# Optimization experiments

Hardware: AMD Instinct MI355X
Metric: run time of the kernel (lower is better)

Reference implementation:

```python
import jax, jax.numpy as jnp
import numpy as np

N_NODES = 50000
N_EDGES = 800000
HID = 256
OUT = 128
NEG_SLOPE = 0.2


def gat_layer(x, src, dst, W_src, W_dst, a_src_vec, a_dst_vec, bias, n_nodes):
    # Dense projections (PyG lin_src / lin_dst for tuple in_channels)
    h_src = x @ W_src              # [N, C]
    h_dst = x @ W_dst              # [N, C]
    # Per-node attention logits (att_src/att_dst dot products)
    a_src = h_src @ a_src_vec      # [N]
    a_dst = h_dst @ a_dst_vec      # [N]
    # Edge logits + LeakyReLU
    e = jax.nn.leaky_relu(a_src[src] + a_dst[dst], NEG_SLOPE)  # [E]
    # Segment softmax over incoming edges of each dst node
    m = jax.ops.segment_max(e, dst, num_segments=n_nodes)      # [N]
    m = jnp.where(jnp.isfinite(m), m, 0.0)                      # empty segments
    ex = jnp.exp(e - m[dst])                                    # [E]
    s = jax.ops.segment_sum(ex, dst, num_segments=n_nodes)     # [N]
    alpha = ex / (s[dst] + 1e-16)                               # [E]
    # Attention-weighted message aggregation (scatter-add to dst)
    msg = alpha[:, None] * h_src[src]                           # [E, C]
    out = jax.ops.segment_sum(msg, dst, num_segments=n_nodes)  # [N, C]
    return out + bias


def setup_inputs() -> dict:
    key = jax.random.key(0)
    ks = jax.random.split(key, 12)
    x = jax.random.normal(ks[0], (N_NODES, HID), dtype=jnp.float32)
    edge_index = jax.random.randint(ks[1], (2, N_EDGES), 0, N_NODES, dtype=jnp.int64)
    sc1 = 1.0 / np.sqrt(HID)
    sc2 = 1.0 / np.sqrt(HID)
    return {
        "x": x,
        "edge_index": edge_index,
        "W1_src": jax.random.normal(ks[2], (HID, HID), dtype=jnp.float32) * sc1,
        "W1_dst": jax.random.normal(ks[3], (HID, HID), dtype=jnp.float32) * sc1,
        "att1_src": jax.random.normal(ks[4], (HID,), dtype=jnp.float32) * sc1,
        "att1_dst": jax.random.normal(ks[5], (HID,), dtype=jnp.float32) * sc1,
        "b1": jnp.zeros((HID,), dtype=jnp.float32),
        "W2_src": jax.random.normal(ks[6], (HID, OUT), dtype=jnp.float32) * sc2,
        "W2_dst": jax.random.normal(ks[7], (HID, OUT), dtype=jnp.float32) * sc2,
        "att2_src": jax.random.normal(ks[8], (OUT,), dtype=jnp.float32) * (1.0 / np.sqrt(OUT)),
        "att2_dst": jax.random.normal(ks[9], (OUT,), dtype=jnp.float32) * (1.0 / np.sqrt(OUT)),
        "b2": jnp.zeros((OUT,), dtype=jnp.float32),
    }


def reference(x, edge_index, W1_src, W1_dst, att1_src, att1_dst, b1,
              W2_src, W2_dst, att2_src, att2_dst, b2):
    src, dst = edge_index[0], edge_index[1]
    h = gat_layer(x, src, dst, W1_src, W1_dst, att1_src, att1_dst, b1, N_NODES)
    h = jax.nn.relu(h)
    out = gat_layer(h, src, dst, W2_src, W2_dst, att2_src, att2_dst, b2, N_NODES)
    return out
```

## Files before the change

### kernel.cpp

```cpp
#include <hip/hip_runtime.h>
#include <math.h>

#define N_NODES 50000
#define N_EDGES 800000
#define HID 256
#define OUT_C 128
#define NEG_SLOPE 0.2f
#define SCAN_NB ((N_NODES + 255) / 256)

typedef __attribute__((ext_vector_type(8))) short bf16x8;
typedef __attribute__((ext_vector_type(4))) float f32x4;
typedef _Float16 half_t;
typedef __attribute__((ext_vector_type(4))) _Float16 half4;
typedef __attribute__((ext_vector_type(2))) _Float16 half2t;

__device__ inline unsigned short bf16_rne(float x) {
    unsigned u = __float_as_uint(x);
    return (unsigned short)((u + 0x7fffu + ((u >> 16) & 1u)) >> 16);
}


__global__ __launch_bounds__(256) void hist_rank_kernel(
    const int* __restrict__ dst, int* __restrict__ counts, int* __restrict__ rank) {
    int e = blockIdx.x * 256 + threadIdx.x;
    if (e < N_EDGES) rank[e] = atomicAdd(&counts[dst[e]], 1);
}

__global__ __launch_bounds__(256) void block_scan_kernel(
    const int* __restrict__ counts, int* __restrict__ excl,
    int* __restrict__ blockSums, int n) {
    __shared__ int waveSums[4];
    int i = blockIdx.x * 256 + threadIdx.x;
    int lane = threadIdx.x & 63;
    int wv = threadIdx.x >> 6;
    int c = (i < n) ? counts[i] : 0;
    int v = c;
    #pragma unroll
    for (int off = 1; off < 64; off <<= 1) {
        int t = __shfl_up(v, off);
        if (lane >= off) v += t;
    }
    if (lane == 63) waveSums[wv] = v;
    __syncthreads();
    int waveOff = 0;
    #pragma unroll
    for (int w = 0; w < 4; w++)
        if (w < wv) waveOff += waveSums[w];
    if (i < n) excl[i] = waveOff + v - c;
    if (threadIdx.x == 255) blockSums[blockIdx.x] = waveOff + v;
}

__global__ __launch_bounds__(256) void add_offsets_kernel(
    int* __restrict__ excl, const int* __restrict__ blockSums, int n) {
    __shared__ int lds[4];
    int tid = threadIdx.x;
    int partial = 0;
    for (int j = tid; j < (int)blockIdx.x; j += 256) partial += blockSums[j];
    #pragma unroll
    for (int off = 32; off > 0; off >>= 1) partial += __shfl_down(partial, off);
    if ((tid & 63) == 0) lds[tid >> 6] = partial;
    __syncthreads();
    int prefix = lds[0] + lds[1] + lds[2] + lds[3];
    int i = blockIdx.x * 256 + tid;
    if (i < n) excl[i] += prefix;
    if (i == 0) excl[n] = N_EDGES;
}

__global__ __launch_bounds__(256) void scatter_kernel(
    const int* __restrict__ src, const int* __restrict__ dst,
    const int* __restrict__ offsets, const int* __restrict__ rank,
    int* __restrict__ src_sorted) {
    int e = blockIdx.x * 256 + threadIdx.x;
    if (e >= N_EDGES) return;
    src_sorted[offsets[dst[e]] + rank[e]] = src[e];
}


__global__ __launch_bounds__(64) void compute_v_all_kernel(
    const float* __restrict__ W1s, const float* __restrict__ att1s,
    const float* __restrict__ W1d, const float* __restrict__ att1d,
    const float* __restrict__ W2s, const float* __restrict__ att2s,
    const float* __restrict__ W2d, const float* __restrict__ att2d,
    float* __restrict__ v1s, float* __restrict__ v1d,
    float* __restrict__ v2s, float* __restrict__ v2d) {
    int k = blockIdx.x;
    int lane = threadIdx.x;
    const float* W; const float* att; float* v; int cout;
    switch (blockIdx.y) {
        case 0: W = W1s; att = att1s; v = v1s; cout = HID; break;
        case 1: W = W1d; att = att1d; v = v1d; cout = HID; break;
        case 2: W = W2s; att = att2s; v = v2s; cout = OUT_C; break;
        default: W = W2d; att = att2d; v = v2d; cout = OUT_C; break;
    }
    float sum = 0.f;
    for (int j = lane; j < cout; j += 64)
        sum += W[k * cout + j] * att[j];
    #pragma unroll
    for (int off = 32; off > 0; off >>= 1)
        sum += __shfl_down(sum, off);
    if (lane == 0) v[k] = sum;
}


#define PACK1_T (8 * 17 * 64)
#define PACK2_T (8 * 9 * 64)

__global__ __launch_bounds__(256) void pack_all_kernel(
    const float* __restrict__ W1, const float* __restrict__ v1s, const float* __restrict__ v1d,
    const float* __restrict__ W2, const float* __restrict__ v2s, const float* __restrict__ v2d,
    unsigned short* __restrict__ hi1, unsigned short* __restrict__ lo1,
    unsigned short* __restrict__ hi2, unsigned short* __restrict__ lo2) {
    int t = blockIdx.x * 256 + threadIdx.x;
    const float *W, *vs, *vd; unsigned short *hi, *lo; int cout, NTL, tt;
    if (t < PACK1_T)            { tt = t;           W = W1; vs = v1s; vd = v1d; hi = hi1; lo = lo1; cout = HID;  NTL = 17; }
    else if (t < PACK1_T + PACK2_T) { tt = t - PACK1_T; W = W2; vs = v2s; vd = v2d; hi = hi2; lo = lo2; cout = OUT_C; NTL = 9; }
    else return;
    int lane = tt & 63;
    int tile = (tt >> 6) % NTL;
    int ks = tt / (64 * NTL);
    int m = lane & 15;
    int kbase = ks * 32 + (lane >> 4) * 8;
    #pragma unroll
    for (int j = 0; j < 8; j++) {
        float val;
        if (tile < NTL - 1) val = W[(kbase + j) * cout + tile * 16 + m];
        else val = (m == 0) ? vs[kbase + j] : (m == 1) ? vd[kbase + j] : 0.f;
        unsigned short h = bf16_rne(val);
        hi[tt * 8 + j] = h;
        lo[tt * 8 + j] = bf16_rne(val - __uint_as_float((unsigned)h << 16));
    }
}


template <int COUT, int NT, bool WRITE_A>
__device__ __forceinline__ void gemm_body(
    const float* __restrict__ A, const unsigned short* __restrict__ Bhi,
    const unsigned short* __restrict__ Blo, half_t* __restrict__ H,
    float* __restrict__ a_s, float* __restrict__ a_d, int M, int tile0) {
    const int NTL = COUT / 16 + 1;
    int wave = threadIdx.x >> 6, lane = threadIdx.x & 63;
    int m = lane & 15, quad = lane >> 4;
    int row0 = blockIdx.x * 128 + wave * 32;
    f32x4 acc[2][NT];
    #pragma unroll
    for (int rg = 0; rg < 2; rg++)
        #pragma unroll
        for (int nt = 0; nt < NT; nt++)
            acc[rg][nt] = (f32x4){0.f, 0.f, 0.f, 0.f};

    const float* arow[2];
    #pragma unroll
    for (int rg = 0; rg < 2; rg++) {
        int r = row0 + rg * 16 + m;
        if (r >= M) r = M - 1;
        arow[rg] = A + (size_t)r * HID;
    }

    for (int ks = 0; ks < 8; ks++) {
        bf16x8 ah[2], al[2];
        #pragma unroll
        for (int rg = 0; rg < 2; rg++) {
            const float* ap = arow[rg] + ks * 32 + quad * 8;
            float4 v0 = *(const float4*)ap;
            float4 v1 = *(const float4*)(ap + 4);
            float av[8] = {v0.x, v0.y, v0.z, v0.w, v1.x, v1.y, v1.z, v1.w};
            #pragma unroll
            for (int j = 0; j < 8; j++) {
                unsigned short h = bf16_rne(av[j]);
                float hf = __uint_as_float((unsigned)h << 16);
                ah[rg][j] = (short)h;
                al[rg][j] = (short)bf16_rne(av[j] - hf);
            }
        }
        #pragma unroll
        for (int nt = 0; nt < NT; nt++) {
            int tile = (WRITE_A && nt == NT - 1) ? (COUT / 16) : (tile0 + nt);
            size_t fbase = ((size_t)(ks * NTL + tile) * 64 + lane) * 8;
            bf16x8 bh = *(const bf16x8*)(Bhi + fbase);
            bf16x8 bl = *(const bf16x8*)(Blo + fbase);
            acc[0][nt] = __builtin_amdgcn_mfma_f32_16x16x32_bf16(ah[0], bh, acc[0][nt], 0, 0, 0);
            acc[1][nt] = __builtin_amdgcn_mfma_f32_16x16x32_bf16(ah[1], bh, acc[1][nt], 0, 0, 0);
            acc[0][nt] = __builtin_amdgcn_mfma_f32_16x16x32_bf16(ah[0], bl, acc[0][nt], 0, 0, 0);
            acc[1][nt] = __builtin_amdgcn_mfma_f32_16x16x32_bf16(ah[1], bl, acc[1][nt], 0, 0, 0);
            acc[0][nt] = __builtin_amdgcn_mfma_f32_16x16x32_bf16(al[0], bh, acc[0][nt], 0, 0, 0);
            acc[1][nt] = __builtin_amdgcn_mfma_f32_16x16x32_bf16(al[1], bh, acc[1][nt], 0, 0, 0);
        }
    }
    const int NW = WRITE_A ? NT - 1 : NT;
    #pragma unroll
    for (int rg = 0; rg < 2; rg++)
        #pragma unroll
        for (int nt = 0; nt < NW; nt++)
            #pragma unroll
            for (int r = 0; r < 4; r++) {
                int row = row0 + rg * 16 + quad * 4 + r;
                if (row < M)
                    H[(size_t)row * COUT + (tile0 + nt) * 16 + m] = (half_t)acc[rg][nt][r];
            }
    if (WRITE_A) {
        #pragma unroll
        for (int rg = 0; rg < 2; rg++)
            #pragma unroll
            for (int r = 0; r < 4; r++) {
                int row = row0 + rg * 16 + quad * 4 + r;
                if (row < M) {
                    if (m == 0) a_s[row] = acc[rg][NT - 1][r];
                    else if (m == 1) a_d[row] = acc[rg][NT - 1][r];
                }
            }
    }
}

template <int COUT>
__global__ __launch_bounds__(256) void mfma_gemm_a_kernel(
    const float* __restrict__ A, const unsigned short* __restrict__ Bhi,
    const unsigned short* __restrict__ Blo, half_t* __restrict__ H,
    float* __restrict__ a_s, float* __restrict__ a_d, int M) {
    if (blockIdx.y == 0)
        gemm_body<COUT, 9, true>(A, Bhi, Blo, H, a_s, a_d, M, 0);
    else
        gemm_body<COUT, 8, false>(A, Bhi, Blo, H, a_s, a_d, M, 8);
}


template <int C, bool RELU>
__global__ __launch_bounds__(256) void fused_aggregate_kernel(
    const int* __restrict__ offsets, const int* __restrict__ src_sorted,
    const float* __restrict__ a_src, const float* __restrict__ a_dst,
    const half_t* __restrict__ h, const float* __restrict__ bias,
    float* __restrict__ out) {
    constexpr int CH = 8;
    int node = (int)((blockIdx.x * 256u + threadIdx.x) >> 6);
    int lane = threadIdx.x & 63;
    if (node >= N_NODES) return;
    int beg = offsets[node], end = offsets[node + 1];
    float ad = a_dst[node];
    float s = 0.f;

    if (C == 256) {
        float4 acc = make_float4(0.f, 0.f, 0.f, 0.f);
        for (int base = beg; base < end; base += CH) {
            int cnt = end - base; if (cnt > CH) cnt = CH;
            int idx[CH];
            #pragma unroll
            for (int j = 0; j < CH; j++)
                idx[j] = src_sorted[(j < cnt) ? base + j : base];
            half4 hv[CH];
            #pragma unroll
            for (int j = 0; j < CH; j++)
                hv[j] = *(const half4*)(h + (size_t)idx[j] * C + lane * 4);
            float w[CH];
            #pragma unroll
            for (int j = 0; j < CH; j++) {
                float l = a_src[idx[j]] + ad;
                if (l < 0.f) l *= NEG_SLOPE;
                w[j] = (j < cnt) ? expf(l) : 0.f;
                s += w[j];
            }
            #pragma unroll
            for (int j = 0; j < CH; j++) {
                acc.x += w[j] * (float)hv[j][0]; acc.y += w[j] * (float)hv[j][1];
                acc.z += w[j] * (float)hv[j][2]; acc.w += w[j] * (float)hv[j][3];
            }
        }
        float inv = 1.f / (s + 1e-16f);
        float4 bv = *(const float4*)(bias + lane * 4);
        acc.x = acc.x * inv + bv.x; acc.y = acc.y * inv + bv.y;
        acc.z = acc.z * inv + bv.z; acc.w = acc.w * inv + bv.w;
        if (RELU) {
            acc.x = fmaxf(acc.x, 0.f); acc.y = fmaxf(acc.y, 0.f);
            acc.z = fmaxf(acc.z, 0.f); acc.w = fmaxf(acc.w, 0.f);
        }
        *(float4*)(out + (size_t)node * C + lane * 4) = acc;
    } else {
        float2 acc = make_float2(0.f, 0.f);
        for (int base = beg; base < end; base += CH) {
            int cnt = end - base; if (cnt > CH) cnt = CH;
            int idx[CH];
            #pragma unroll
            for (int j = 0; j < CH; j++)
                idx[j] = src_sorted[(j < cnt) ? base + j : base];
            half2t hv[CH];
            #pragma unroll
            for (int j = 0; j < CH; j++)
                hv[j] = *(const half2t*)(h + (size_t)idx[j] * C + lane * 2);
            float w[CH];
            #pragma unroll
            for (int j = 0; j < CH; j++) {
                float l = a_src[idx[j]] + ad;
                if (l < 0.f) l *= NEG_SLOPE;
                w[j] = (j < cnt) ? expf(l) : 0.f;
                s += w[j];
            }
            #pragma unroll
            for (int j = 0; j < CH; j++) {
                acc.x += w[j] * (float)hv[j][0]; acc.y += w[j] * (float)hv[j][1];
            }
        }
        float inv = 1.f / (s + 1e-16f);
        float2 bv = *(const float2*)(bias + lane * 2);
        acc.x = acc.x * inv + bv.x; acc.y = acc.y * inv + bv.y;
        if (RELU) { acc.x = fmaxf(acc.x, 0.f); acc.y = fmaxf(acc.y, 0.f); }
        *(float2*)(out + (size_t)node * C + lane * 2) = acc;
    }
}

extern "C" void kernel_launch(void* const* d_in, const int* in_sizes, int n_in,
                              void* d_out, int out_size, void* d_ws, size_t ws_size,
                              hipStream_t stream) {
    const float* x     = (const float*)d_in[0];
    const int*   edge  = (const int*)d_in[1];
    const int*   src   = edge;
    const int*   dst   = edge + N_EDGES;
    const float* W1s   = (const float*)d_in[2];
    const float* W1d   = (const float*)d_in[3];
    const float* att1s = (const float*)d_in[4];
    const float* att1d = (const float*)d_in[5];
    const float* b1    = (const float*)d_in[6];
    const float* W2s   = (const float*)d_in[7];
    const float* W2d   = (const float*)d_in[8];
    const float* att2s = (const float*)d_in[9];
    const float* att2d = (const float*)d_in[10];
    const float* b2    = (const float*)d_in[11];
    float* out = (float*)d_out;

    float* ws    = (float*)d_ws;
    half_t* h1   = (half_t*)ws;
    float* act2  = ws + (size_t)N_NODES * HID;
    float* a_s   = act2 + (size_t)N_NODES * HID;
    float* a_d   = a_s + N_NODES;
    float* vbuf  = a_d + N_NODES;
    int* ibase      = (int*)(vbuf + 4 * HID);
    int* src_sorted = ibase;
    int* rank       = src_sorted + N_EDGES;
    int* counts     = rank + N_EDGES;
    int* offsets    = counts + N_NODES;
    int* blockSums  = offsets + N_NODES + 1;
    unsigned short* wp1h = (unsigned short*)(((uintptr_t)(blockSums + SCAN_NB) + 15) & ~(uintptr_t)15);
    unsigned short* wp1l = wp1h + PACK1_T * 8;
    unsigned short* wp2h = wp1l + PACK1_T * 8;
    unsigned short* wp2l = wp2h + PACK2_T * 8;
    float* v1s = vbuf, *v1d = vbuf + HID, *v2s = vbuf + 2 * HID, *v2d = vbuf + 3 * HID;
    half_t* h2 = h1;

    const int edgeBlocks = (N_EDGES + 255) / 256;
    const int waveBlocksN = (N_NODES + 3) / 4;
    const int gemmBlocks = (N_NODES + 127) / 128;

    hipMemsetAsync(counts, 0, N_NODES * sizeof(int), stream);
    hist_rank_kernel<<<edgeBlocks, 256, 0, stream>>>(dst, counts, rank);
    block_scan_kernel<<<SCAN_NB, 256, 0, stream>>>(counts, offsets, blockSums, N_NODES);
    add_offsets_kernel<<<SCAN_NB, 256, 0, stream>>>(offsets, blockSums, N_NODES);
    scatter_kernel<<<edgeBlocks, 256, 0, stream>>>(src, dst, offsets, rank, src_sorted);

    compute_v_all_kernel<<<dim3(HID, 4), 64, 0, stream>>>(
        W1s, att1s, W1d, att1d, W2s, att2s, W2d, att2d, v1s, v1d, v2s, v2d);
    pack_all_kernel<<<(PACK1_T + PACK2_T + 255) / 256, 256, 0, stream>>>(
        W1s, v1s, v1d, W2s, v2s, v2d, wp1h, wp1l, wp2h, wp2l);

    mfma_gemm_a_kernel<HID><<<dim3(gemmBlocks, 2), 256, 0, stream>>>(
        x, wp1h, wp1l, h1, a_s, a_d, N_NODES);
    fused_aggregate_kernel<HID, true><<<waveBlocksN, 256, 0, stream>>>(
        offsets, src_sorted, a_s, a_d, h1, b1, act2);

    mfma_gemm_a_kernel<OUT_C><<<dim3(gemmBlocks, 1), 256, 0, stream>>>(
        act2, wp2h, wp2l, h2, a_s, a_d, N_NODES);
    fused_aggregate_kernel<OUT_C, false><<<waveBlocksN, 256, 0, stream>>>(
        offsets, src_sorted, a_s, a_d, h2, b2, out);
}
```

Before: 339.6 us.

## Precompute per-edge softmax weights in separate kernel before aggregation

Adds an edge-parallel kernel that computes exp(leaky_relu(a_src[src]+a_dst[dst])) for every sorted edge, and stores dst_sorted during the CSR scatter so that kernel can find each edge's target. The aggregation kernels then read contiguous weights instead of gathering a_src and computing exp per wave. Padding the sorted arrays by 8 zero entries lets the index loads drop their bounds clamp. In exchange it adds two extra launches and extra global traffic for dst_sorted and the weight array, and switches to the faster, less accurate __expf.

```diff
diff --git a/kernel.cpp b/kernel.cpp
--- a/kernel.cpp
+++ b/kernel.cpp
@@ -69,10 +69,13 @@
 __global__ __launch_bounds__(256) void scatter_kernel(
     const int* __restrict__ src, const int* __restrict__ dst,
     const int* __restrict__ offsets, const int* __restrict__ rank,
-    int* __restrict__ src_sorted) {
+    int* __restrict__ src_sorted, int* __restrict__ dst_sorted) {
     int e = blockIdx.x * 256 + threadIdx.x;
     if (e >= N_EDGES) return;
-    src_sorted[offsets[dst[e]] + rank[e]] = src[e];
+    int pos = offsets[dst[e]] + rank[e];
+    src_sorted[pos] = src[e];
+    dst_sorted[pos] = dst[e];
+    if (e < 8) { src_sorted[N_EDGES + e] = 0; dst_sorted[N_EDGES + e] = 0; }
 }
 
 
@@ -223,28 +226,38 @@
 }
 
 
+__global__ __launch_bounds__(256) void exw_kernel(
+    const int* __restrict__ src_sorted, const int* __restrict__ dst_sorted,
+    const float* __restrict__ a_src, const float* __restrict__ a_dst,
+    float* __restrict__ exs) {
+    int e = blockIdx.x * 256 + threadIdx.x;
+    if (e >= N_EDGES) return;
+    float l = a_src[src_sorted[e]] + a_dst[dst_sorted[e]];
+    if (l < 0.f) l *= NEG_SLOPE;
+    exs[e] = __expf(l);
+}
+
+
 template <int C, bool RELU>
 __global__ __launch_bounds__(256) void fused_aggregate_kernel(
     const int* __restrict__ offsets, const int* __restrict__ src_sorted,
-    const float* __restrict__ a_src, const float* __restrict__ a_dst,
-    const half_t* __restrict__ h, const float* __restrict__ bias,
-    float* __restrict__ out) {
+    const float* __restrict__ exs, const half_t* __restrict__ h,
+    const float* __restrict__ bias, float* __restrict__ out) {
     constexpr int CH = 8;
     int node = (int)((blockIdx.x * 256u + threadIdx.x) >> 6);
     int lane = threadIdx.x & 63;
     if (node >= N_NODES) return;
     int beg = offsets[node], end = offsets[node + 1];
-    float ad = a_dst[node];
     float s = 0.f;
 
     if (C == 256) {
         float4 acc = make_float4(0.f, 0.f, 0.f, 0.f);
         for (int base = beg; base < end; base += CH) {
-            int cnt = end - base; if (cnt > CH) cnt = CH;
+            int cnt = end - base;
             int idx[CH];
             #pragma unroll
             for (int j = 0; j < CH; j++)
-                idx[j] = src_sorted[(j < cnt) ? base + j : base];
+                idx[j] = src_sorted[base + j];
             half4 hv[CH];
             #pragma unroll
             for (int j = 0; j < CH; j++)
@@ -252,9 +265,7 @@
             float w[CH];
             #pragma unroll
             for (int j = 0; j < CH; j++) {
-                float l = a_src[idx[j]] + ad;
-                if (l < 0.f) l *= NEG_SLOPE;
-                w[j] = (j < cnt) ? expf(l) : 0.f;
+                w[j] = (j < cnt) ? exs[base + j] : 0.f;
                 s += w[j];
             }
             #pragma unroll
@@ -275,11 +286,11 @@
     } else {
         float2 acc = make_float2(0.f, 0.f);
         for (int base = beg; base < end; base += CH) {
-            int cnt = end - base; if (cnt > CH) cnt = CH;
+            int cnt = end - base;
             int idx[CH];
             #pragma unroll
             for (int j = 0; j < CH; j++)
-                idx[j] = src_sorted[(j < cnt) ? base + j : base];
+                idx[j] = src_sorted[base + j];
             half2t hv[CH];
             #pragma unroll
             for (int j = 0; j < CH; j++)
@@ -287,9 +298,7 @@
             float w[CH];
             #pragma unroll
             for (int j = 0; j < CH; j++) {
-                float l = a_src[idx[j]] + ad;
-                if (l < 0.f) l *= NEG_SLOPE;
-                w[j] = (j < cnt) ? expf(l) : 0.f;
+                w[j] = (j < cnt) ? exs[base + j] : 0.f;
                 s += w[j];
             }
             #pragma unroll
@@ -329,10 +338,12 @@
     float* act2  = ws + (size_t)N_NODES * HID;
     float* a_s   = act2 + (size_t)N_NODES * HID;
     float* a_d   = a_s + N_NODES;
-    float* vbuf  = a_d + N_NODES;
+    float* exs   = a_d + N_NODES;
+    float* vbuf  = exs + N_EDGES + 8;
     int* ibase      = (int*)(vbuf + 4 * HID);
     int* src_sorted = ibase;
-    int* rank       = src_sorted + N_EDGES;
+    int* dst_sorted = src_sorted + N_EDGES + 8;
+    int* rank       = dst_sorted + N_EDGES + 8;
     int* counts     = rank + N_EDGES;
     int* offsets    = counts + N_NODES;
     int* blockSums  = offsets + N_NODES + 1;
@@ -351,7 +362,7 @@
     hist_rank_kernel<<<edgeBlocks, 256, 0, stream>>>(dst, counts, rank);
     block_scan_kernel<<<SCAN_NB, 256, 0, stream>>>(counts, offsets, blockSums, N_NODES);
     add_offsets_kernel<<<SCAN_NB, 256, 0, stream>>>(offsets, blockSums, N_NODES);
-    scatter_kernel<<<edgeBlocks, 256, 0, stream>>>(src, dst, offsets, rank, src_sorted);
+    scatter_kernel<<<edgeBlocks, 256, 0, stream>>>(src, dst, offsets, rank, src_sorted, dst_sorted);
 
     compute_v_all_kernel<<<dim3(HID, 4), 64, 0, stream>>>(
         W1s, att1s, W1d, att1d, W2s, att2s, W2d, att2d, v1s, v1d, v2s, v2d);
@@ -360,11 +371,13 @@
 
     mfma_gemm_a_kernel<HID><<<dim3(gemmBlocks, 2), 256, 0, stream>>>(
         x, wp1h, wp1l, h1, a_s, a_d, N_NODES);
+    exw_kernel<<<edgeBlocks, 256, 0, stream>>>(src_sorted, dst_sorted, a_s, a_d, exs);
     fused_aggregate_kernel<HID, true><<<waveBlocksN, 256, 0, stream>>>(
-        offsets, src_sorted, a_s, a_d, h1, b1, act2);
+        offsets, src_sorted, exs, h1, b1, act2);
 
     mfma_gemm_a_kernel<OUT_C><<<dim3(gemmBlocks, 1), 256, 0, stream>>>(
         act2, wp2h, wp2l, h2, a_s, a_d, N_NODES);
+    exw_kernel<<<edgeBlocks, 256, 0, stream>>>(src_sorted, dst_sorted, a_s, a_d, exs);
     fused_aggregate_kernel<OUT_C, false><<<waveBlocksN, 256, 0, stream>>>(
-        offsets, src_sorted, a_s, a_d, h2, b2, out);
-}
+        offsets, src_sorted, exs, h2, b2, out);
+}
```

Result: slower. 351.8 us (+3.6%).
